# Performance work log

Measured on AMD Instinct MI355X. Metric: run time of the kernel, lower is better.

## Reference

```python
import jax, jax.numpy as jnp
import numpy as np

B, S, E_DIM, H_DIM, WID, HGT = 64, 128, 256, 128, 64, 64


def setup_inputs() -> dict:
    key = jax.random.key(0)
    k1, k2, k3, k4 = jax.random.split(key, 4)
    e = jax.random.normal(k1, (B, S, E_DIM), dtype=jnp.float32)
    h = jax.random.normal(k2, (B, H_DIM, WID, HGT), dtype=jnp.float32)
    W = jax.random.normal(k3, (H_DIM, E_DIM), dtype=jnp.float32) * (1.0 / np.sqrt(E_DIM))
    b = jax.random.normal(k4, (H_DIM,), dtype=jnp.float32) * 0.01
    return {"e": e, "h": h, "W": W, "b": b}


def reference(e, h, W, b):
    # Linear: (B, S, e_dim) -> (B, S, h_dim)
    ep = jnp.einsum('bse,de->bsd', e, W) + b
    batch, ch, width, height = h.shape
    hv = h.reshape(batch, ch, width * height)          # (B, D, N)
    # scores s = bmm(e^T_proj, h): (B, S, N)
    s = jnp.einsum('bsd,bdn->bsn', ep, hv)
    # softmax over seq dim (dim=1 in torch)
    beta = jax.nn.softmax(s, axis=1)
    # c = sum_s e[b,d,s] * beta[b,s,n]  -> (B, D, N)  (true batched GEMM)
    c = jnp.einsum('bsd,bsn->bdn', ep, beta)
    return c.reshape(batch, ch, width, height)
```

## Files before the change

### kernel.cpp

```cpp
#include <hip/hip_runtime.h>
#include <math.h>

#define B_ 64
#define S_ 128
#define E_ 256
#define D_ 128
#define N_ 4096

typedef _Float16 f16;
typedef _Float16 f16x8 __attribute__((ext_vector_type(8)));
typedef float f32x4 __attribute__((ext_vector_type(4)));

__device__ __forceinline__ unsigned pack2(f16 a, f16 b) {
    union { f16 h[2]; unsigned u; } x;
    x.h[0] = a; x.h[1] = b; return x.u;
}

__device__ __forceinline__ f32x4 mfma16(f16x8 a, f16x8 b, f32x4 c) {
    return __builtin_amdgcn_mfma_f32_16x16x32_f16(a, b, c, 0, 0, 0);
}

__device__ __forceinline__ void bar_lds() {
    asm volatile("s_waitcnt lgkmcnt(0)" ::: "memory");
    __builtin_amdgcn_s_barrier();
    asm volatile("" ::: "memory");
}

__global__ __launch_bounds__(256) void k1_ep(
    const float* __restrict__ e, const float* __restrict__ W,
    const float* __restrict__ bias,
    unsigned* __restrict__ epA_h, unsigned* __restrict__ epA_l,
    unsigned* __restrict__ epT_h)
{
    __shared__ __align__(16) unsigned char lds[40960];
    f16* ehB = (f16*)lds;
    f16* elB = (f16*)(lds + 4096);
    f16* WhB = (f16*)(lds + 8192);
    f16* WlB = (f16*)(lds + 24576);

    const int t = threadIdx.x;
    const int b  = blockIdx.x >> 2;
    const int s0 = (blockIdx.x & 3) << 5;
    const int wid = t >> 6, lane = t & 63;
    const int l16 = lane & 15, quad = lane >> 4;

    const int se = t >> 3, e8 = t & 7;
    const int dw = t >> 1, half = t & 1;
    const float* egp = e + (size_t)(b * S_ + s0 + se) * E_ + e8 * 8;
    const float* wgp = W + (size_t)dw * E_ + half * 32;
    const int eoff = (se * 128 + e8 * 16) ^ ((se & 7) << 4);
    const int woffb = dw * 128 + half * 64;
    const int wswz = (dw & 7) << 4;

    float4 ve[2], vw[8];
#define K1_LOAD(KC)                                            \
    do {                                                       \
        ve[0] = *(const float4*)(egp + (KC));                  \
        ve[1] = *(const float4*)(egp + (KC) + 4);              \
        _Pragma("unroll")                                      \
        for (int x = 0; x < 8; ++x)                            \
            vw[x] = *(const float4*)(wgp + (KC) + x * 4);      \
    } while (0)

    K1_LOAD(0);

    f32x4 acc[2][2];
#pragma unroll
    for (int mt = 0; mt < 2; ++mt)
#pragma unroll
        for (int nt = 0; nt < 2; ++nt) acc[mt][nt] = (f32x4)0.f;

#pragma unroll 1
    for (int kc = 0; kc < 4; ++kc) {
        {
            f16x8 vh, vl;
#pragma unroll
            for (int x = 0; x < 8; ++x) {
                const float v = (x < 4) ? ((const float*)&ve[0])[x]
                                        : ((const float*)&ve[1])[x - 4];
                const f16 h_ = (f16)v;
                vh[x] = h_; vl[x] = (f16)(v - (float)h_);
            }
            *(f16x8*)((char*)ehB + eoff) = vh;
            *(f16x8*)((char*)elB + eoff) = vl;
        }
#pragma unroll
        for (int g = 0; g < 4; ++g) {
            f16x8 vh, vl;
#pragma unroll
            for (int x = 0; x < 8; ++x) {
                const float v = (x < 4) ? ((const float*)&vw[2 * g])[x]
                                        : ((const float*)&vw[2 * g + 1])[x - 4];
                const f16 h_ = (f16)v;
                vh[x] = h_; vl[x] = (f16)(v - (float)h_);
            }
            const int off = (woffb + g * 16) ^ wswz;
            *(f16x8*)((char*)WhB + off) = vh;
            *(f16x8*)((char*)WlB + off) = vl;
        }
        if (kc < 3) K1_LOAD((kc + 1) * 64);
        bar_lds();

#pragma unroll
        for (int kke = 0; kke < 2; ++kke) {
            const int ebyte = kke * 64 + quad * 16;
            f16x8 ah[2], al[2], bh[2], bl[2];
#pragma unroll
            for (int mt = 0; mt < 2; ++mt) {
                const int row = mt * 16 + l16;
                const int off = (row * 128 + ebyte) ^ ((row & 7) << 4);
                ah[mt] = *(const f16x8*)((const char*)ehB + off);
                al[mt] = *(const f16x8*)((const char*)elB + off);
            }
#pragma unroll
            for (int nt = 0; nt < 2; ++nt) {
                const int dr = (wid << 5) + nt * 16 + l16;
                const int off = (dr * 128 + ebyte) ^ ((dr & 7) << 4);
                bh[nt] = *(const f16x8*)((const char*)WhB + off);
                bl[nt] = *(const f16x8*)((const char*)WlB + off);
            }
#pragma unroll
            for (int mt = 0; mt < 2; ++mt)
#pragma unroll
                for (int nt = 0; nt < 2; ++nt) {
                    acc[mt][nt] = mfma16(ah[mt], bh[nt], acc[mt][nt]);
                    acc[mt][nt] = mfma16(ah[mt], bl[nt], acc[mt][nt]);
                    acc[mt][nt] = mfma16(al[mt], bh[nt], acc[mt][nt]);
                }
        }
        bar_lds();
    }
#undef K1_LOAD

    f16 hi[2][2][4], lo[2][2][4];
#pragma unroll
    for (int nt = 0; nt < 2; ++nt) {
        const int d = (wid << 5) + nt * 16 + l16;
        const float bz = bias[d];
#pragma unroll
        for (int mt = 0; mt < 2; ++mt)
#pragma unroll
            for (int r = 0; r < 4; ++r) {
                const float val = acc[mt][nt][r] + bz;
                const f16 h_ = (f16)val;
                hi[mt][nt][r] = h_;
                lo[mt][nt][r] = (f16)(val - (float)h_);
            }
    }

#pragma unroll
    for (int mt = 0; mt < 2; ++mt)
#pragma unroll
        for (int nt = 0; nt < 2; ++nt) {
            const int d = (wid << 5) + nt * 16 + l16;
            const int sg = s0 + mt * 16 + quad * 4;
            unsigned* p = epT_h + (size_t)(b * D_ + d) * 64 + (sg >> 1);
            p[0] = pack2(hi[mt][nt][0], hi[mt][nt][1]);
            p[1] = pack2(hi[mt][nt][2], hi[mt][nt][3]);
        }

    f16* oAh = (f16*)lds;
    f16* oAl = (f16*)(lds + 8704);
#pragma unroll
    for (int mt = 0; mt < 2; ++mt)
#pragma unroll
        for (int nt = 0; nt < 2; ++nt)
#pragma unroll
            for (int r = 0; r < 4; ++r) {
                const int sl = mt * 16 + quad * 4 + r;
                const int d = (wid << 5) + nt * 16 + l16;
                oAh[sl * 136 + d] = hi[mt][nt][r];
                oAl[sl * 136 + d] = lo[mt][nt][r];
            }
    bar_lds();
    {
        const int sl = t >> 3, j8 = (t & 7) * 8;
        const char* rh = (const char*)oAh + sl * 272 + j8 * 4;
        const char* rl = (const char*)oAl + sl * 272 + j8 * 4;
        uint4* dh = (uint4*)(epA_h + (size_t)(b * S_ + s0 + sl) * 64 + j8);
        uint4* dl = (uint4*)(epA_l + (size_t)(b * S_ + s0 + sl) * 64 + j8);
        dh[0] = *(const uint4*)rh; dh[1] = *(const uint4*)(rh + 16);
        dl[0] = *(const uint4*)rl; dl[1] = *(const uint4*)(rl + 16);
    }
}

__global__ __launch_bounds__(256, 3) void k2_attn(
    const float* __restrict__ h, const f16* __restrict__ epA_h,
    const f16* __restrict__ epA_l, const f16* __restrict__ epT_h,
    float* __restrict__ out)
{
    __shared__ __align__(16) unsigned char hTb[32768];
    __shared__ __align__(16) unsigned char bTb[16384];
    __shared__ __align__(16) float redb[256];

    const int phys = blockIdx.x;
    const int L = (phys & 7) * 512 + (phys >> 3);
    const int b  = L >> 6;
    const int n0 = (L & 63) << 6;

    const int t = threadIdx.x;
    const int wid = t >> 6, lane = t & 63;
    const int l16 = lane & 15, quad = lane >> 4;

    const int sn = t & 63;
    float va[32];
    {
        const float* hp = h + (size_t)(b * D_ + (t >> 6) * 32) * N_ + n0 + sn;
#pragma unroll
        for (int x = 0; x < 32; ++x) va[x] = hp[(size_t)x * N_];
    }
    {
        const int swzn = (sn & 15) << 4;
#pragma unroll
        for (int g = 0; g < 4; ++g) {
            f16x8 vh, vl;
#pragma unroll
            for (int x = 0; x < 8; ++x) {
                const float v = va[g * 8 + x];
                const f16 h_ = (f16)v;
                vh[x] = h_; vl[x] = (f16)(v - (float)h_);
            }
            const int off = (sn * 256 + wid * 64 + g * 16) ^ swzn;
            *(f16x8*)(hTb + off) = vh;
            *(f16x8*)(hTb + 16384 + off) = vl;
        }
    }
    bar_lds();

    const int sb = wid << 5;
    f32x4 acc[2][4];
#pragma unroll
    for (int mt = 0; mt < 2; ++mt)
#pragma unroll
        for (int nt = 0; nt < 4; ++nt) acc[mt][nt] = (f32x4)0.f;

    const f16* Ah = epA_h + (size_t)(b * S_ + sb + l16) * D_ + quad * 8;
    const f16* Al = epA_l + (size_t)(b * S_ + sb + l16) * D_ + quad * 8;
#pragma unroll
    for (int kk = 0; kk < 4; ++kk) {
        const int dcb = kk * 64 + quad * 16;
        f16x8 bh[4], bl[4];
#pragma unroll
        for (int nt = 0; nt < 4; ++nt) {
            const int n = (nt << 4) + l16;
            const int off = (n * 256 + dcb) ^ ((n & 15) << 4);
            bh[nt] = *(const f16x8*)(hTb + off);
            bl[nt] = *(const f16x8*)(hTb + 16384 + off);
        }
#pragma unroll
        for (int mt = 0; mt < 2; ++mt) {
            const f16x8 ah = *(const f16x8*)(Ah + mt * 16 * D_ + kk * 32);
            const f16x8 al = *(const f16x8*)(Al + mt * 16 * D_ + kk * 32);
#pragma unroll
            for (int nt = 0; nt < 4; ++nt) {
                acc[mt][nt] = mfma16(ah, bh[nt], acc[mt][nt]);
                acc[mt][nt] = mfma16(ah, bl[nt], acc[mt][nt]);
                acc[mt][nt] = mfma16(al, bh[nt], acc[mt][nt]);
            }
        }
    }

#pragma unroll
    for (int nt = 0; nt < 4; ++nt) {
        float ps = 0.f;
#pragma unroll
        for (int mt = 0; mt < 2; ++mt)
#pragma unroll
            for (int r = 0; r < 4; ++r) {
                const float e_ = __expf(acc[mt][nt][r] - 30.f);
                acc[mt][nt][r] = e_;
                ps += e_;
            }
        ps += __shfl_xor(ps, 16);
        ps += __shfl_xor(ps, 32);
        if (quad == 0) redb[(((nt << 4) + l16) << 2) + wid] = ps;
    }
    bar_lds();

#pragma unroll
    for (int nt = 0; nt < 4; ++nt) {
        const int n = (nt << 4) + l16;
        const f32x4 s4 = *(const f32x4*)(redb + (n << 2));
        const float inv = 1.f / (s4[0] + s4[1] + s4[2] + s4[3]);
#pragma unroll
        for (int mt = 0; mt < 2; ++mt) {
            uint2 pk;
            pk.x = pack2((f16)(acc[mt][nt][0] * inv),
                         (f16)(acc[mt][nt][1] * inv));
            pk.y = pack2((f16)(acc[mt][nt][2] * inv),
                         (f16)(acc[mt][nt][3] * inv));
            const int bo = (n * 256 + wid * 64 + mt * 32 + quad * 8)
                           ^ ((n & 15) << 4);
            *(uint2*)(bTb + bo) = pk;
        }
    }
    bar_lds();

    const int db = wid << 5;
    f32x4 a2[2][4];
#pragma unroll
    for (int mt = 0; mt < 2; ++mt)
#pragma unroll
        for (int nt = 0; nt < 4; ++nt) a2[mt][nt] = (f32x4)0.f;

    const f16* At = epT_h + (size_t)(b * D_ + db + l16) * S_ + quad * 8;
#pragma unroll
    for (int kk = 0; kk < 4; ++kk) {
        const int scb = kk * 64 + quad * 16;
        f16x8 bb[4];
#pragma unroll
        for (int nt = 0; nt < 4; ++nt) {
            const int n = (nt << 4) + l16;
            const int off = (n * 256 + scb) ^ ((n & 15) << 4);
            bb[nt] = *(const f16x8*)(bTb + off);
        }
#pragma unroll
        for (int mt = 0; mt < 2; ++mt) {
            const f16x8 av = *(const f16x8*)(At + mt * 16 * S_ + kk * 32);
#pragma unroll
            for (int nt = 0; nt < 4; ++nt)
                a2[mt][nt] = mfma16(av, bb[nt], a2[mt][nt]);
        }
    }

    float* ob = out + (size_t)(b * D_ + db) * N_ + n0;
#pragma unroll
    for (int mt = 0; mt < 2; ++mt)
#pragma unroll
        for (int nt = 0; nt < 4; ++nt)
#pragma unroll
            for (int r = 0; r < 4; ++r)
                ob[(size_t)(mt * 16 + quad * 4 + r) * N_ + (nt << 4) + l16] =
                    a2[mt][nt][r];
}

extern "C" void kernel_launch(void* const* d_in, const int* in_sizes, int n_in,
                              void* d_out, int out_size, void* d_ws, size_t ws_size,
                              hipStream_t stream) {
    const float* e    = (const float*)d_in[0];
    const float* h    = (const float*)d_in[1];
    const float* W    = (const float*)d_in[2];
    const float* bias = (const float*)d_in[3];
    float* out = (float*)d_out;

    unsigned* epA_h = (unsigned*)d_ws;
    unsigned* epA_l = epA_h + (B_ * S_ * D_ / 2);
    unsigned* epT_h = epA_l + (B_ * S_ * D_ / 2);

    hipLaunchKernelGGL(k1_ep, dim3(B_ * 4), dim3(256), 0, stream,
                       e, W, bias, epA_h, epA_l, epT_h);
    hipLaunchKernelGGL(k2_attn, dim3(B_ * 64), dim3(256), 0, stream,
                       h, (const f16*)epA_h, (const f16*)epA_l,
                       (const f16*)epT_h, out);
}
```

Before: 299.1 us.

## Alias softmax LDS buffers onto h tile and prefetch first A fragments

Reuses the 32KB h-transpose LDS buffer for the softmax column-sum scratch and the beta tile, adding a barrier so the aliased region is only written once all waves finish reading h. Static LDS per block falls from about 49KB to 32KB, and launch bounds go from 3 to 5 blocks per CU to raise occupancy. The first k-slice of the ep_h/ep_l and epT fragments is prefetched from global memory early so its latency overlaps the h conversion and the softmax. The costs are an extra barrier and higher register pressure under the tighter launch bound, which could cause spills.

Measured after the change: 324.7 us. 8.6% more time.

```diff
diff --git a/kernel.cpp b/kernel.cpp
--- a/kernel.cpp
+++ b/kernel.cpp
@@ -184,14 +184,15 @@
     }
 }
 
-__global__ __launch_bounds__(256, 3) void k2_attn(
+__global__ __launch_bounds__(256, 5) void k2_attn(
     const float* __restrict__ h, const f16* __restrict__ epA_h,
     const f16* __restrict__ epA_l, const f16* __restrict__ epT_h,
     float* __restrict__ out)
 {
     __shared__ __align__(16) unsigned char hTb[32768];
-    __shared__ __align__(16) unsigned char bTb[16384];
-    __shared__ __align__(16) float redb[256];
+
+    f16*   bTp  = (f16*)hTb;
+    float* redb = (float*)(hTb + 16384);
 
     const int phys = blockIdx.x;
     const int L = (phys & 7) * 512 + (phys >> 3);
@@ -201,14 +202,24 @@
     const int t = threadIdx.x;
     const int wid = t >> 6, lane = t & 63;
     const int l16 = lane & 15, quad = lane >> 4;
+    const int sb = wid << 5, db = wid << 5;
 
     const int sn = t & 63;
     float va[32];
     {
-        const float* hp = h + (size_t)(b * D_ + (t >> 6) * 32) * N_ + n0 + sn;
+        const float* hp = h + (size_t)(b * D_ + wid * 32) * N_ + n0 + sn;
 #pragma unroll
         for (int x = 0; x < 32; ++x) va[x] = hp[(size_t)x * N_];
     }
+
+    const f16* Ah = epA_h + (size_t)(b * S_ + sb + l16) * D_ + quad * 8;
+    const f16* Al = epA_l + (size_t)(b * S_ + sb + l16) * D_ + quad * 8;
+    f16x8 ah0[2], al0[2];
+    ah0[0] = *(const f16x8*)(Ah);
+    al0[0] = *(const f16x8*)(Al);
+    ah0[1] = *(const f16x8*)(Ah + 16 * D_);
+    al0[1] = *(const f16x8*)(Al + 16 * D_);
+
     {
         const int swzn = (sn & 15) << 4;
 #pragma unroll
@@ -227,15 +238,12 @@
     }
     bar_lds();
 
-    const int sb = wid << 5;
     f32x4 acc[2][4];
 #pragma unroll
     for (int mt = 0; mt < 2; ++mt)
 #pragma unroll
         for (int nt = 0; nt < 4; ++nt) acc[mt][nt] = (f32x4)0.f;
 
-    const f16* Ah = epA_h + (size_t)(b * S_ + sb + l16) * D_ + quad * 8;
-    const f16* Al = epA_l + (size_t)(b * S_ + sb + l16) * D_ + quad * 8;
 #pragma unroll
     for (int kk = 0; kk < 4; ++kk) {
         const int dcb = kk * 64 + quad * 16;
@@ -249,8 +257,10 @@
         }
 #pragma unroll
         for (int mt = 0; mt < 2; ++mt) {
-            const f16x8 ah = *(const f16x8*)(Ah + mt * 16 * D_ + kk * 32);
-            const f16x8 al = *(const f16x8*)(Al + mt * 16 * D_ + kk * 32);
+            const f16x8 ah = (kk == 0) ? ah0[mt]
+                : *(const f16x8*)(Ah + mt * 16 * D_ + kk * 32);
+            const f16x8 al = (kk == 0) ? al0[mt]
+                : *(const f16x8*)(Al + mt * 16 * D_ + kk * 32);
 #pragma unroll
             for (int nt = 0; nt < 4; ++nt) {
                 acc[mt][nt] = mfma16(ah, bh[nt], acc[mt][nt]);
@@ -260,21 +270,31 @@
         }
     }
 
+    const f16* At = epT_h + (size_t)(b * D_ + db + l16) * S_ + quad * 8;
+    f16x8 av0[2];
+    av0[0] = *(const f16x8*)(At);
+    av0[1] = *(const f16x8*)(At + 16 * S_);
+
+    float ps[4];
 #pragma unroll
     for (int nt = 0; nt < 4; ++nt) {
-        float ps = 0.f;
+        float p = 0.f;
 #pragma unroll
         for (int mt = 0; mt < 2; ++mt)
 #pragma unroll
             for (int r = 0; r < 4; ++r) {
                 const float e_ = __expf(acc[mt][nt][r] - 30.f);
                 acc[mt][nt][r] = e_;
-                ps += e_;
-            }
-        ps += __shfl_xor(ps, 16);
-        ps += __shfl_xor(ps, 32);
-        if (quad == 0) redb[(((nt << 4) + l16) << 2) + wid] = ps;
-    }
+                p += e_;
+            }
+        p += __shfl_xor(p, 16);
+        p += __shfl_xor(p, 32);
+        ps[nt] = p;
+    }
+    bar_lds();
+#pragma unroll
+    for (int nt = 0; nt < 4; ++nt)
+        if (quad == 0) redb[(((nt << 4) + l16) << 2) + wid] = ps[nt];
     bar_lds();
 
 #pragma unroll
@@ -291,19 +311,17 @@
                          (f16)(acc[mt][nt][3] * inv));
             const int bo = (n * 256 + wid * 64 + mt * 32 + quad * 8)
                            ^ ((n & 15) << 4);
-            *(uint2*)(bTb + bo) = pk;
-        }
-    }
-    bar_lds();
-
-    const int db = wid << 5;
+            *(uint2*)((char*)bTp + bo) = pk;
+        }
+    }
+    bar_lds();
+
     f32x4 a2[2][4];
 #pragma unroll
     for (int mt = 0; mt < 2; ++mt)
 #pragma unroll
         for (int nt = 0; nt < 4; ++nt) a2[mt][nt] = (f32x4)0.f;
 
-    const f16* At = epT_h + (size_t)(b * D_ + db + l16) * S_ + quad * 8;
 #pragma unroll
     for (int kk = 0; kk < 4; ++kk) {
         const int scb = kk * 64 + quad * 16;
@@ -312,11 +330,12 @@
         for (int nt = 0; nt < 4; ++nt) {
             const int n = (nt << 4) + l16;
             const int off = (n * 256 + scb) ^ ((n & 15) << 4);
-            bb[nt] = *(const f16x8*)(bTb + off);
+            bb[nt] = *(const f16x8*)((const char*)bTp + off);
         }
 #pragma unroll
         for (int mt = 0; mt < 2; ++mt) {
-            const f16x8 av = *(const f16x8*)(At + mt * 16 * S_ + kk * 32);
+            const f16x8 av = (kk == 0) ? av0[mt]
+                : *(const f16x8*)(At + mt * 16 * S_ + kk * 32);
 #pragma unroll
             for (int nt = 0; nt < 4; ++nt)
                 a2[mt][nt] = mfma16(av, bb[nt], a2[mt][nt]);
```
